# Kernel optimization log

Measured on AMD Instinct MI355X. Metric: run time of the kernel, lower is better.

Reference implementation:

```python
import jax, jax.numpy as jnp
import numpy as np

NUM_HEADS = 16


def setup_inputs() -> dict:
    key = jax.random.key(0)
    ks = jax.random.split(key, 6)
    B, N, L, C = 2, 1024, 4096, 1024
    x_obj = jax.random.normal(ks[0], (B, N, C), dtype=jnp.float32)
    x_ctx = jax.random.normal(ks[1], (B, L, C), dtype=jnp.float32)
    s = 1.0 / np.sqrt(C)
    Wq = jax.random.normal(ks[2], (C, C), dtype=jnp.float32) * s
    Wkv = jax.random.normal(ks[3], (C, 2 * C), dtype=jnp.float32) * s
    Wproj = jax.random.normal(ks[4], (C, C), dtype=jnp.float32) * s
    bproj = jax.random.normal(ks[5], (C,), dtype=jnp.float32) * 0.01
    return {"x_obj": x_obj, "x_ctx": x_ctx, "Wq": Wq, "Wkv": Wkv,
            "Wproj": Wproj, "bproj": bproj}


def _split_heads(t, H):
    # [B, T, C] -> [B, H, T, d]
    B, T, C = t.shape
    return t.reshape(B, T, H, C // H).transpose(0, 2, 1, 3)


def reference(x_obj, x_ctx, Wq, Wkv, Wproj, bproj):
    B, N, C = x_obj.shape
    H = NUM_HEADS
    d = C // H
    scale = d ** -0.5

    q = _split_heads(x_obj @ Wq, H)                      # [B,H,N,d]

    kv_o = x_obj @ Wkv                                   # [B,N,2C] -> (2,H,d) split
    k_obj = _split_heads(kv_o[..., :C], H)               # [B,H,N,d]
    v_obj = _split_heads(kv_o[..., C:], H)

    kv_c = x_ctx @ Wkv                                   # [B,L,2C]
    k_ctx = _split_heads(kv_c[..., :C], H)               # [B,H,L,d]
    v_ctx = _split_heads(kv_c[..., C:], H)

    k = jnp.concatenate([k_obj, k_ctx], axis=2)          # [B,H,N+L,d]
    v = jnp.concatenate([v_obj, v_ctx], axis=2)

    attn = jnp.einsum('bhnd,bhmd->bhnm', q, k) * scale   # [B,H,N,N+L]
    attn = jax.nn.softmax(attn, axis=-1)
    out = jnp.einsum('bhnm,bhmd->bhnd', attn, v)         # [B,H,N,d]
    out = out.transpose(0, 2, 1, 3).reshape(B, N, C)
    return out @ Wproj + bproj
```

## Files before the change

kernel.cpp:

```cpp
#include <hip/hip_runtime.h>
#include <stdint.h>

typedef unsigned short u16;
typedef unsigned int   u32;
typedef __attribute__((ext_vector_type(8))) short bf16x8;
typedef __attribute__((ext_vector_type(4))) float f32x4;

__device__ __forceinline__ u16 f2bf(float f) {
    union { float f; u32 u; } v; v.f = f;
    return (u16)((v.u + 0x7FFFu + ((v.u >> 16) & 1u)) >> 16);
}
__device__ __forceinline__ float bf2f(u16 h) {
    union { u32 u; float f; } v; v.u = ((u32)h) << 16; return v.f;
}
__device__ __forceinline__ u32 fbits(float f) {
    union { float f; u32 u; } v; v.f = f; return v.u;
}

__device__ __forceinline__ void async16(const u16* g, u16* l) {
    typedef __attribute__((address_space(1))) const u32 gq;
    typedef __attribute__((address_space(3))) u32 lq;
    __builtin_amdgcn_global_load_lds((gq*)g, (lq*)l, 16, 0, 0);
}

__global__ void cvt_all_k(const float* __restrict__ xo, const float* __restrict__ xc,
                          u16* __restrict__ Xc,
                          const float* __restrict__ Wq, const float* __restrict__ Wkv,
                          const float* __restrict__ Wp,
                          u16* __restrict__ Wqt, u16* __restrict__ Wkt,
                          u16* __restrict__ Wpt)
{
    __shared__ __align__(16) u16 Ts[64][72];
    int id = blockIdx.x, t = threadIdx.x;
    if (id < 10240) {
        int row = id, cid = t * 4;
        int b = row >= 5120, s = row - b * 5120;
        const float* src = (s < 1024)
            ? xo + ((size_t)(b * 1024 + s)) * 1024 + cid
            : xc + ((size_t)(b * 4096 + s - 1024)) * 1024 + cid;
        float4 f = *(const float4*)src;
        union { u16 a[4]; uint2 v; } p;
        p.a[0]=f2bf(f.x); p.a[1]=f2bf(f.y); p.a[2]=f2bf(f.z); p.a[3]=f2bf(f.w);
        *(uint2*)(Xc + (size_t)row * 1024 + cid) = p.v;
        return;
    }
    int wid = id - 10240;
    const float* W; u16* Wt; int N, tile;
    if (wid < 256)      { W = Wq;  Wt = Wqt; N = 1024; tile = wid; }
    else if (wid < 768) { W = Wkv; Wt = Wkt; N = 2048; tile = wid - 256; }
    else                { W = Wp;  Wt = Wpt; N = 1024; tile = wid - 768; }
    int nt = N >> 6;
    int n0 = (tile % nt) * 64, k0 = (tile / nt) * 64;
    int lr = t >> 2, lc = (t & 3) * 16;
    const float* src = W + (size_t)(k0 + lr) * N + n0 + lc;
    union { u16 a[8]; uint4 v; } p0, p1;
    float4 f0 = *(const float4*)(src),      f1 = *(const float4*)(src + 4);
    float4 f2 = *(const float4*)(src + 8),  f3 = *(const float4*)(src + 12);
    p0.a[0]=f2bf(f0.x); p0.a[1]=f2bf(f0.y); p0.a[2]=f2bf(f0.z); p0.a[3]=f2bf(f0.w);
    p0.a[4]=f2bf(f1.x); p0.a[5]=f2bf(f1.y); p0.a[6]=f2bf(f1.z); p0.a[7]=f2bf(f1.w);
    p1.a[0]=f2bf(f2.x); p1.a[1]=f2bf(f2.y); p1.a[2]=f2bf(f2.z); p1.a[3]=f2bf(f2.w);
    p1.a[4]=f2bf(f3.x); p1.a[5]=f2bf(f3.y); p1.a[6]=f2bf(f3.z); p1.a[7]=f2bf(f3.w);
    *(uint4*)&Ts[lr][lc]     = p0.v;
    *(uint4*)&Ts[lr][lc + 8] = p1.v;
    __syncthreads();
    union { u16 a[8]; uint4 v; } q0, q1;
#pragma unroll
    for (int j = 0; j < 8; ++j) q0.a[j] = Ts[lc + j][lr];
#pragma unroll
    for (int j = 0; j < 8; ++j) q1.a[j] = Ts[lc + 8 + j][lr];
    u16* dst = Wt + (size_t)(n0 + lr) * 1024 + k0 + lc;
    *(uint4*)dst       = q0.v;
    *(uint4*)(dst + 8) = q1.v;
}

__global__ __launch_bounds__(256, 2)
void gemm_qkv(const u16* __restrict__ A, const u16* __restrict__ Wqt,
              const u16* __restrict__ Wkt, u16* __restrict__ q,
              u16* __restrict__ Kh, u16* __restrict__ Vh)
{
    __shared__ __align__(16) u16 smem[17408];
    u16* As = smem;
    u16* Bs = smem + 4096;

    const int t = threadIdx.x, w = t >> 6;
    const int lane = t & 63, quad = lane >> 4, l16 = lane & 15;
    const int id = blockIdx.x;
    const bool qm = id >= 1280;
    int m0, n0; const u16* Bt;
    if (qm) { int t2 = id - 1280; m0 = (t2 >> 3) * 128; n0 = (t2 & 7) * 128; Bt = Wqt; }
    else    { m0 = (id >> 4) * 128; n0 = (id & 15) * 128; Bt = Wkt; }
    const int wr = (w >> 1) * 64, wc = (w & 1) * 64;

    const int sr0 = w * 32 + (lane >> 2), sr1 = sr0 + 16;
    const int cg  = (lane & 3) ^ ((lane >> 4) & 3);
    u16* abase = As + w * 1024;
    u16* bbase = Bs + w * 1024;

    const u16 *ar0, *ar1;
    {
        int g0 = m0 + sr0, g1 = m0 + sr1;
        if (qm) {
            ar0 = A + ((size_t)(g0 >> 10) * 5120 + (g0 & 1023)) * 1024;
            ar1 = A + ((size_t)(g1 >> 10) * 5120 + (g1 & 1023)) * 1024;
        } else {
            ar0 = A + (size_t)g0 * 1024;
            ar1 = A + (size_t)g1 * 1024;
        }
        ar0 += cg * 8; ar1 += cg * 8;
    }
    const u16* br0 = Bt + (size_t)(n0 + sr0) * 1024 + cg * 8;
    const u16* br1 = Bt + (size_t)(n0 + sr1) * 1024 + cg * 8;

    f32x4 acc[4][4] = {};
    const int sel = (quad ^ (l16 >> 2)) * 8;

    for (int k0 = 0; k0 < 1024; k0 += 32) {
        async16(ar0 + k0, abase);
        async16(ar1 + k0, abase + 512);
        async16(br0 + k0, bbase);
        async16(br1 + k0, bbase + 512);
        __syncthreads();

        bf16x8 av[4], bv[4];
#pragma unroll
        for (int i = 0; i < 4; ++i)
            av[i] = *(const bf16x8*)&As[(wr + i * 16 + l16) * 32 + sel];
#pragma unroll
        for (int j = 0; j < 4; ++j)
            bv[j] = *(const bf16x8*)&Bs[(wc + j * 16 + l16) * 32 + sel];
#pragma unroll
        for (int i = 0; i < 4; ++i)
#pragma unroll
            for (int j = 0; j < 4; ++j)
                acc[i][j] = __builtin_amdgcn_mfma_f32_16x16x32_bf16(av[i], bv[j], acc[i][j], 0, 0, 0);
        __syncthreads();
    }

    if (qm) {
        const float SC = 0.180336880f;
#pragma unroll
        for (int j = 0; j < 4; ++j) {
            int col = n0 + wc + j * 16 + l16;
#pragma unroll
            for (int i = 0; i < 4; ++i) {
                int rowb = m0 + wr + i * 16 + quad * 4;
#pragma unroll
                for (int r = 0; r < 4; ++r)
                    q[(size_t)(rowb + r) * 1024 + col] = f2bf(acc[i][j][r] * SC);
            }
        }
        return;
    }
    int b = m0 >= 5120;
    int keyb = m0 - b * 5120;
    if (n0 < 1024) {
#pragma unroll
        for (int j = 0; j < 4; ++j) {
            int col = n0 + wc + j * 16 + l16;
#pragma unroll
            for (int i = 0; i < 4; ++i) {
                int rowb = m0 + wr + i * 16 + quad * 4;
                int key = rowb - b * 5120;
                int bh = b * 16 + (col >> 6), d = col & 63;
                u16* dst = Kh + ((size_t)bh * 5120 + key) * 64 + d;
#pragma unroll
                for (int r = 0; r < 4; ++r) dst[r * 64] = f2bf(acc[i][j][r]);
            }
        }
    } else {
        u16* T = smem;
#pragma unroll
        for (int j = 0; j < 4; ++j) {
            int d2 = wc + j * 16 + l16;
#pragma unroll
            for (int i = 0; i < 4; ++i) {
                int kl = wr + i * 16 + quad * 4;
                union { u16 a[4]; uint2 v; } pk;
#pragma unroll
                for (int r = 0; r < 4; ++r) pk.a[r] = f2bf(acc[i][j][r]);
                *(uint2*)&T[d2 * 136 + kl] = pk.v;
            }
        }
        __syncthreads();
        int hb = (n0 - 1024) >> 6;
#pragma unroll
        for (int p = 0; p < 8; ++p) {
            int idx = p * 256 + t;
            int d2 = idx >> 4, k0c = (idx & 15) * 8;
            uint4 vv = *(const uint4*)&T[d2 * 136 + k0c];
            int bh = b * 16 + hb + (d2 >> 6), d = d2 & 63;
            *(uint4*)(Vh + ((size_t)bh * 64 + d) * 5120 + keyb + k0c) = vv;
        }
    }
}

__global__ __launch_bounds__(256, 2)
void gemm_proj(const u16* __restrict__ A, const u16* __restrict__ Bt,
               const float* __restrict__ bias, float* __restrict__ Cf)
{
    __shared__ __align__(16) u16 As[128 * 32];
    __shared__ __align__(16) u16 Bs[64 * 32];

    const int t = threadIdx.x, w = t >> 6;
    const int lane = t & 63, quad = lane >> 4, l16 = lane & 15;
    const int m0 = blockIdx.y * 128, n0 = blockIdx.x * 64;
    const int wr = w * 32;

    const int sr0 = w * 32 + (lane >> 2), sr1 = sr0 + 16;
    const int cg  = (lane & 3) ^ ((lane >> 4) & 3);
    u16* abase = As + w * 1024;
    u16* bbase = Bs + w * 512;

    const u16* ar0 = A + (size_t)(m0 + sr0) * 1024 + cg * 8;
    const u16* ar1 = A + (size_t)(m0 + sr1) * 1024 + cg * 8;
    const u16* br0 = Bt + (size_t)(n0 + w * 16 + (lane >> 2)) * 1024 + cg * 8;

    f32x4 acc[2][4] = {};
    const int sel = (quad ^ (l16 >> 2)) * 8;

    for (int k0 = 0; k0 < 1024; k0 += 32) {
        async16(ar0 + k0, abase);
        async16(ar1 + k0, abase + 512);
        async16(br0 + k0, bbase);
        __syncthreads();

        bf16x8 av[2], bv[4];
#pragma unroll
        for (int i = 0; i < 2; ++i)
            av[i] = *(const bf16x8*)&As[(wr + i * 16 + l16) * 32 + sel];
#pragma unroll
        for (int j = 0; j < 4; ++j)
            bv[j] = *(const bf16x8*)&Bs[(j * 16 + l16) * 32 + sel];
#pragma unroll
        for (int i = 0; i < 2; ++i)
#pragma unroll
            for (int j = 0; j < 4; ++j)
                acc[i][j] = __builtin_amdgcn_mfma_f32_16x16x32_bf16(av[i], bv[j], acc[i][j], 0, 0, 0);
        __syncthreads();
    }

#pragma unroll
    for (int j = 0; j < 4; ++j) {
        int col = n0 + j * 16 + l16;
        float bvl = bias[col];
#pragma unroll
        for (int i = 0; i < 2; ++i) {
            int rowb = m0 + wr + i * 16 + quad * 4;
#pragma unroll
            for (int r = 0; r < 4; ++r)
                Cf[(size_t)(rowb + r) * 1024 + col] = acc[i][j][r] + bvl;
        }
    }
}

__global__ __launch_bounds__(256, 4)
void attn_k(const u16* __restrict__ Q, const u16* __restrict__ Kh,
            const u16* __restrict__ Vh, u16* __restrict__ Op,
            float* __restrict__ Lp)
{
    __shared__ __align__(16) u16 Ks[4096];
    __shared__ __align__(16) u16 Vt[4096];
    __shared__ __align__(16) u16 Ps[8192];

    const int tid  = threadIdx.x;
    const int wave = tid >> 6, lane = tid & 63;
    const int quad = lane >> 4, l16 = lane & 15;
    const int bx = blockIdx.x;
    const int part = bx & 3, qt = (bx >> 2) & 7, h = (bx >> 5) & 15, b = bx >> 9;
    const int bh = b * 16 + h;

    const int qrow0 = b * 1024 + qt * 128 + wave * 32;
    const u16* qbase = Q + (size_t)qrow0 * 1024 + h * 64;

    bf16x8 aq[2][2];
#pragma unroll
    for (int rt = 0; rt < 2; ++rt) {
        aq[rt][0] = *(const bf16x8*)(qbase + (size_t)(rt * 16 + l16) * 1024 +      quad * 8);
        aq[rt][1] = *(const bf16x8*)(qbase + (size_t)(rt * 16 + l16) * 1024 + 32 + quad * 8);
    }

    union { u32 u[4]; bf16x8 v; } onesf;
#pragma unroll
    for (int i = 0; i < 4; ++i) onesf.u[i] = 0x3F803F80u;

    f32x4 o[2][4] = {};
    f32x4 lacc[2] = {};

    const u16* kbase = Kh + (size_t)bh * 5120 * 64;
    const u16* vbase = Vh + (size_t)bh * 64 * 5120;
    const int srow = tid >> 2;
    const int scg  = (tid & 3) * 2;
    const int m7   = srow & 7;
    const int l7   = l16 & 7;
    u16* kdst0 = Ks + srow * 64 + ((scg ^ m7) * 8);
    u16* kdst1 = Ks + srow * 64 + (((scg + 1) ^ m7) * 8);
    u16* vdst0 = Vt + srow * 64 + ((scg ^ m7) * 8);
    u16* vdst1 = Vt + srow * 64 + (((scg + 1) ^ m7) * 8);
    u16* psw   = Ps + wave * 2048;
    const int m_beg = part * 1280;

    for (int c = 0; c < 20; ++c) {
        const int m0 = m_beg + c * 64;
        {
            const u16* ks = kbase + (size_t)(m0 + srow) * 64 + scg * 8;
            *(uint4*)kdst0 = *(const uint4*)(ks);
            *(uint4*)kdst1 = *(const uint4*)(ks + 8);
        }
        {
            const u16* vs = vbase + (size_t)srow * 5120 + m0 + (tid & 3) * 4;
            uint2 g0 = *(const uint2*)(vs);
            uint2 g1 = *(const uint2*)(vs + 16);
            uint2 g2 = *(const uint2*)(vs + 32);
            uint2 g3 = *(const uint2*)(vs + 48);
            uint4 o0, o1;
            o0.x = __builtin_amdgcn_perm(g1.x, g0.x, 0x05040100u);
            o0.y = __builtin_amdgcn_perm(g3.x, g2.x, 0x05040100u);
            o0.z = __builtin_amdgcn_perm(g1.x, g0.x, 0x07060302u);
            o0.w = __builtin_amdgcn_perm(g3.x, g2.x, 0x07060302u);
            o1.x = __builtin_amdgcn_perm(g1.y, g0.y, 0x05040100u);
            o1.y = __builtin_amdgcn_perm(g3.y, g2.y, 0x05040100u);
            o1.z = __builtin_amdgcn_perm(g1.y, g0.y, 0x07060302u);
            o1.w = __builtin_amdgcn_perm(g3.y, g2.y, 0x07060302u);
            *(uint4*)vdst0 = o0;
            *(uint4*)vdst1 = o1;
        }
        __syncthreads();

        f32x4 s[2][4] = {};
#pragma unroll
        for (int nt = 0; nt < 4; ++nt) {
            const u16* krow = Ks + (nt * 16 + l16) * 64;
            bf16x8 kb0 = *(const bf16x8*)(krow + ((quad     ^ l7) * 8));
            bf16x8 kb1 = *(const bf16x8*)(krow + (((4+quad) ^ l7) * 8));
#pragma unroll
            for (int rt = 0; rt < 2; ++rt) {
                s[rt][nt] = __builtin_amdgcn_mfma_f32_16x16x32_bf16(aq[rt][0], kb0, s[rt][nt], 0, 0, 0);
                s[rt][nt] = __builtin_amdgcn_mfma_f32_16x16x32_bf16(aq[rt][1], kb1, s[rt][nt], 0, 0, 0);
            }
        }

#pragma unroll
        for (int rt = 0; rt < 2; ++rt)
#pragma unroll
            for (int r = 0; r < 4; ++r) {
                float e0 = exp2f(s[rt][0][r]);
                float e1 = exp2f(s[rt][1][r]);
                float e2 = exp2f(s[rt][2][r]);
                float e3 = exp2f(s[rt][3][r]);
                uint2 pw;
                pw.x = __builtin_amdgcn_perm(fbits(e1), fbits(e0), 0x07060302u);
                pw.y = __builtin_amdgcn_perm(fbits(e3), fbits(e2), 0x07060302u);
                int qr = quad * 4 + r;
                *(uint2*)(psw + (rt * 16 + qr) * 64 +
                          (((l16 >> 1) ^ (qr & 7)) * 8) + (l16 & 1) * 4) = pw;
            }

        asm volatile("s_waitcnt lgkmcnt(0)" ::: "memory");

        bf16x8 pf[2][2];
#pragma unroll
        for (int rt = 0; rt < 2; ++rt) {
            const u16* prow = psw + (rt * 16 + l16) * 64;
            pf[rt][0] = *(const bf16x8*)(prow + ((quad     ^ l7) * 8));
            pf[rt][1] = *(const bf16x8*)(prow + (((4+quad) ^ l7) * 8));
        }

#pragma unroll
        for (int rt = 0; rt < 2; ++rt) {
            lacc[rt] = __builtin_amdgcn_mfma_f32_16x16x32_bf16(pf[rt][0], onesf.v, lacc[rt], 0, 0, 0);
            lacc[rt] = __builtin_amdgcn_mfma_f32_16x16x32_bf16(pf[rt][1], onesf.v, lacc[rt], 0, 0, 0);
        }

#pragma unroll
        for (int dt = 0; dt < 4; ++dt) {
            const u16* vrow = Vt + (dt * 16 + l16) * 64;
            bf16x8 v0 = *(const bf16x8*)(vrow + ((quad     ^ l7) * 8));
            bf16x8 v1 = *(const bf16x8*)(vrow + (((4+quad) ^ l7) * 8));
#pragma unroll
            for (int rt = 0; rt < 2; ++rt) {
                o[rt][dt] = __builtin_amdgcn_mfma_f32_16x16x32_bf16(pf[rt][0], v0, o[rt][dt], 0, 0, 0);
                o[rt][dt] = __builtin_amdgcn_mfma_f32_16x16x32_bf16(pf[rt][1], v1, o[rt][dt], 0, 0, 0);
            }
        }
        __syncthreads();
    }

    const int Rb = bh * 1024 + qt * 128 + wave * 32;
    u16* obase = Op + ((size_t)part << 21);
#pragma unroll
    for (int rt = 0; rt < 2; ++rt)
#pragma unroll
        for (int dt = 0; dt < 4; ++dt)
#pragma unroll
            for (int r = 0; r < 4; ++r) {
                int R = Rb + rt * 16 + quad * 4 + r;
                obase[(size_t)R * 64 + dt * 16 + l16] = f2bf(o[rt][dt][r]);
            }
    if (l16 == 0) {
#pragma unroll
        for (int rt = 0; rt < 2; ++rt)
#pragma unroll
            for (int r = 0; r < 4; ++r)
                Lp[part * 32768 + Rb + rt * 16 + quad * 4 + r] = lacc[rt][r];
    }
}

__global__ void comb_k(const u16* __restrict__ Op, const float* __restrict__ Lp,
                       u16* __restrict__ ao)
{
    int t = blockIdx.x * 256 + threadIdx.x;
    int R = t >> 4, dg = (t & 15) * 4;
    float l = Lp[R] + Lp[32768 + R] + Lp[65536 + R] + Lp[98304 + R];
    float a[4] = {0.f, 0.f, 0.f, 0.f};
#pragma unroll
    for (int p = 0; p < 4; ++p) {
        union { u16 a[4]; uint2 v; } w;
        w.v = *(const uint2*)(Op + ((size_t)p << 21) + (size_t)R * 64 + dg);
#pragma unroll
        for (int j = 0; j < 4; ++j) a[j] += bf2f(w.a[j]);
    }
    float inv = 1.f / l;
    int bh = R >> 10, n = R & 1023, b = bh >> 4, h = bh & 15;
    union { u16 a[4]; uint2 v; } out;
#pragma unroll
    for (int j = 0; j < 4; ++j) out.a[j] = f2bf(a[j] * inv);
    *(uint2*)(ao + (size_t)(b * 1024 + n) * 1024 + h * 64 + dg) = out.v;
}

extern "C" void kernel_launch(void* const* d_in, const int* in_sizes, int n_in,
                              void* d_out, int out_size, void* d_ws, size_t ws_size,
                              hipStream_t stream)
{
    const float* x_obj = (const float*)d_in[0];
    const float* x_ctx = (const float*)d_in[1];
    const float* Wq    = (const float*)d_in[2];
    const float* Wkv   = (const float*)d_in[3];
    const float* Wproj = (const float*)d_in[4];
    const float* bproj = (const float*)d_in[5];
    float* out = (float*)d_out;

    u16* Xc  = (u16*)d_ws;
    u16* ao  = Xc;
    u16* Op  = Xc + (size_t)2097152;
    u16* Wqt = Xc  + (size_t)10485760;
    u16* Wkt = Wqt + (size_t)1048576;
    u16* Wpt = Wkt + (size_t)2097152;
    u16* q   = Wpt + (size_t)1048576;
    u16* Kh  = q   + (size_t)2097152;
    u16* Vh  = Kh  + (size_t)10485760;
    float* Lp = (float*)(Vh + (size_t)10485760);

    dim3 blk(256);
    cvt_all_k<<<dim3(11264), blk, 0, stream>>>(x_obj, x_ctx, Xc,
                                               Wq, Wkv, Wproj, Wqt, Wkt, Wpt);
    gemm_qkv<<<dim3(1408), blk, 0, stream>>>(Xc, Wqt, Wkt, q, Kh, Vh);
    attn_k<<<dim3(1024), blk, 0, stream>>>(q, Kh, Vh, Op, Lp);
    comb_k<<<dim3(2048), blk, 0, stream>>>(Op, Lp, ao);
    gemm_proj<<<dim3(16, 16), blk, 0, stream>>>(ao, Wpt, bproj, out);
}
```

Before: 256.2 us.

## Split attention KV range into five parts and prefetch next K/V tile into registers

The attention kernel now splits the key/value range into five 1024-key partitions instead of four 1280-key ones, giving 1280 blocks. The block index is reordered so the partition is the outermost index, and the occupancy hint is raised to 5 blocks per CU. Global loads for the next K/V tile are issued into registers before the compute on the current tile, so memory latency overlaps with the MFMA work. MFMA sections are wrapped in s_setprio, and the combine kernel sums five partials. The extra partial output reuses the now-dead Wq/Wk workspace, which costs more combine traffic and adds register pressure under the tighter launch bound.

```diff
diff --git a/kernel.cpp b/kernel.cpp
--- a/kernel.cpp
+++ b/kernel.cpp
@@ -253,7 +253,7 @@
     }
 }
 
-__global__ __launch_bounds__(256, 4)
+__global__ __launch_bounds__(256, 5)
 void attn_k(const u16* __restrict__ Q, const u16* __restrict__ Kh,
             const u16* __restrict__ Vh, u16* __restrict__ Op,
             float* __restrict__ Lp)
@@ -266,7 +266,9 @@
     const int wave = tid >> 6, lane = tid & 63;
     const int quad = lane >> 4, l16 = lane & 15;
     const int bx = blockIdx.x;
-    const int part = bx & 3, qt = (bx >> 2) & 7, h = (bx >> 5) & 15, b = bx >> 9;
+    const int part = bx >> 8;
+    const int rest = bx & 255;
+    const int qt = rest & 7, h = (rest >> 3) & 15, b = rest >> 7;
     const int bh = b * 16 + h;
 
     const int qrow0 = b * 1024 + qt * 128 + wave * 32;
@@ -297,36 +299,47 @@
     u16* vdst0 = Vt + srow * 64 + ((scg ^ m7) * 8);
     u16* vdst1 = Vt + srow * 64 + (((scg + 1) ^ m7) * 8);
     u16* psw   = Ps + wave * 2048;
-    const int m_beg = part * 1280;
-
-    for (int c = 0; c < 20; ++c) {
-        const int m0 = m_beg + c * 64;
+    const int m_beg = part * 1024;
+
+    const u16* kptr = kbase + (size_t)(m_beg + srow) * 64 + scg * 8;
+    const u16* vptr = vbase + (size_t)srow * 5120 + m_beg + (tid & 3) * 4;
+    uint4 kr0 = *(const uint4*)kptr;
+    uint4 kr1 = *(const uint4*)(kptr + 8);
+    uint2 vg0 = *(const uint2*)(vptr);
+    uint2 vg1 = *(const uint2*)(vptr + 16);
+    uint2 vg2 = *(const uint2*)(vptr + 32);
+    uint2 vg3 = *(const uint2*)(vptr + 48);
+
+    for (int c = 0; c < 16; ++c) {
+        *(uint4*)kdst0 = kr0;
+        *(uint4*)kdst1 = kr1;
         {
-            const u16* ks = kbase + (size_t)(m0 + srow) * 64 + scg * 8;
-            *(uint4*)kdst0 = *(const uint4*)(ks);
-            *(uint4*)kdst1 = *(const uint4*)(ks + 8);
-        }
-        {
-            const u16* vs = vbase + (size_t)srow * 5120 + m0 + (tid & 3) * 4;
-            uint2 g0 = *(const uint2*)(vs);
-            uint2 g1 = *(const uint2*)(vs + 16);
-            uint2 g2 = *(const uint2*)(vs + 32);
-            uint2 g3 = *(const uint2*)(vs + 48);
             uint4 o0, o1;
-            o0.x = __builtin_amdgcn_perm(g1.x, g0.x, 0x05040100u);
-            o0.y = __builtin_amdgcn_perm(g3.x, g2.x, 0x05040100u);
-            o0.z = __builtin_amdgcn_perm(g1.x, g0.x, 0x07060302u);
-            o0.w = __builtin_amdgcn_perm(g3.x, g2.x, 0x07060302u);
-            o1.x = __builtin_amdgcn_perm(g1.y, g0.y, 0x05040100u);
-            o1.y = __builtin_amdgcn_perm(g3.y, g2.y, 0x05040100u);
-            o1.z = __builtin_amdgcn_perm(g1.y, g0.y, 0x07060302u);
-            o1.w = __builtin_amdgcn_perm(g3.y, g2.y, 0x07060302u);
+            o0.x = __builtin_amdgcn_perm(vg1.x, vg0.x, 0x05040100u);
+            o0.y = __builtin_amdgcn_perm(vg3.x, vg2.x, 0x05040100u);
+            o0.z = __builtin_amdgcn_perm(vg1.x, vg0.x, 0x07060302u);
+            o0.w = __builtin_amdgcn_perm(vg3.x, vg2.x, 0x07060302u);
+            o1.x = __builtin_amdgcn_perm(vg1.y, vg0.y, 0x05040100u);
+            o1.y = __builtin_amdgcn_perm(vg3.y, vg2.y, 0x05040100u);
+            o1.z = __builtin_amdgcn_perm(vg1.y, vg0.y, 0x07060302u);
+            o1.w = __builtin_amdgcn_perm(vg3.y, vg2.y, 0x07060302u);
             *(uint4*)vdst0 = o0;
             *(uint4*)vdst1 = o1;
         }
+        if (c < 15) {
+            kptr += 4096;
+            vptr += 64;
+            kr0 = *(const uint4*)kptr;
+            kr1 = *(const uint4*)(kptr + 8);
+            vg0 = *(const uint2*)(vptr);
+            vg1 = *(const uint2*)(vptr + 16);
+            vg2 = *(const uint2*)(vptr + 32);
+            vg3 = *(const uint2*)(vptr + 48);
+        }
         __syncthreads();
 
         f32x4 s[2][4] = {};
+        __builtin_amdgcn_s_setprio(1);
 #pragma unroll
         for (int nt = 0; nt < 4; ++nt) {
             const u16* krow = Ks + (nt * 16 + l16) * 64;
@@ -338,6 +351,7 @@
                 s[rt][nt] = __builtin_amdgcn_mfma_f32_16x16x32_bf16(aq[rt][1], kb1, s[rt][nt], 0, 0, 0);
             }
         }
+        __builtin_amdgcn_s_setprio(0);
 
 #pragma unroll
         for (int rt = 0; rt < 2; ++rt)
@@ -365,6 +379,7 @@
             pf[rt][1] = *(const bf16x8*)(prow + (((4+quad) ^ l7) * 8));
         }
 
+        __builtin_amdgcn_s_setprio(1);
 #pragma unroll
         for (int rt = 0; rt < 2; ++rt) {
             lacc[rt] = __builtin_amdgcn_mfma_f32_16x16x32_bf16(pf[rt][0], onesf.v, lacc[rt], 0, 0, 0);
@@ -382,6 +397,7 @@
                 o[rt][dt] = __builtin_amdgcn_mfma_f32_16x16x32_bf16(pf[rt][1], v1, o[rt][dt], 0, 0, 0);
             }
         }
+        __builtin_amdgcn_s_setprio(0);
         __syncthreads();
     }
 
@@ -410,10 +426,10 @@
 {
     int t = blockIdx.x * 256 + threadIdx.x;
     int R = t >> 4, dg = (t & 15) * 4;
-    float l = Lp[R] + Lp[32768 + R] + Lp[65536 + R] + Lp[98304 + R];
+    float l = Lp[R] + Lp[32768 + R] + Lp[65536 + R] + Lp[98304 + R] + Lp[131072 + R];
     float a[4] = {0.f, 0.f, 0.f, 0.f};
 #pragma unroll
-    for (int p = 0; p < 4; ++p) {
+    for (int p = 0; p < 5; ++p) {
         union { u16 a[4]; uint2 v; } w;
         w.v = *(const uint2*)(Op + ((size_t)p << 21) + (size_t)R * 64 + dg);
 #pragma unroll
@@ -448,13 +464,13 @@
     u16* q   = Wpt + (size_t)1048576;
     u16* Kh  = q   + (size_t)2097152;
     u16* Vh  = Kh  + (size_t)10485760;
-    float* Lp = (float*)(Vh + (size_t)10485760);
+    float* Lp = (float*)(Wkt + (size_t)1048576);
 
     dim3 blk(256);
     cvt_all_k<<<dim3(11264), blk, 0, stream>>>(x_obj, x_ctx, Xc,
                                                Wq, Wkv, Wproj, Wqt, Wkt, Wpt);
     gemm_qkv<<<dim3(1408), blk, 0, stream>>>(Xc, Wqt, Wkt, q, Kh, Vh);
-    attn_k<<<dim3(1024), blk, 0, stream>>>(q, Kh, Vh, Op, Lp);
+    attn_k<<<dim3(1280), blk, 0, stream>>>(q, Kh, Vh, Op, Lp);
     comb_k<<<dim3(2048), blk, 0, stream>>>(Op, Lp, ao);
     gemm_proj<<<dim3(16, 16), blk, 0, stream>>>(ao, Wpt, bproj, out);
 }
```

New measurement: 611.0 us. 139% more time.
